# Kernel optimization log

Hardware: AMD Instinct MI355X
Metric: run time of the kernel (lower is better)

## Reference

```python
import jax, jax.numpy as jnp
import numpy as np

N_HEAD = 16
HEAD_DIM = 32          # n_embed // n_head // 2
LAMBDA_INIT = 0.2      # 0.8 - 0.6*exp(-0.3*(layer-1)) with layer=1
ROPE_BASE = 10000.0
EPS = 1e-5


def _rope(x):
    # torchtune RotaryPositionalEmbeddings: interleaved adjacent pairs
    B, T, H, D = x.shape
    half = D // 2
    theta = ROPE_BASE ** (-(jnp.arange(half, dtype=jnp.float32) * 2.0 / D))  # [half]
    ang = jnp.arange(T, dtype=jnp.float32)[:, None] * theta[None, :]         # [T, half]
    cos = jnp.cos(ang)[None, :, None, :]
    sin = jnp.sin(ang)[None, :, None, :]
    xr = x.reshape(B, T, H, half, 2)
    x1, x2 = xr[..., 0], xr[..., 1]
    out = jnp.stack([x1 * cos - x2 * sin, x1 * sin + x2 * cos], axis=-1)
    return out.reshape(B, T, H, D).astype(x.dtype)


def reference(x, W_attn, W_proj, lambda_q1, lambda_k1, lambda_q2, lambda_k2):
    B, T, C = x.shape
    H, D = N_HEAD, HEAD_DIM
    qkv = x @ W_attn                              # [B,T,3C]
    q, k, v = jnp.split(qkv, 3, axis=-1)
    q = _rope(q.reshape(B, T, 2 * H, D)).transpose(0, 2, 1, 3)   # [B,2H,T,D]
    k = _rope(k.reshape(B, T, 2 * H, D)).transpose(0, 2, 1, 3)   # [B,2H,T,D]
    v = v.reshape(B, T, H, 2 * D).transpose(0, 2, 1, 3)          # [B,H,T,2D]

    lam = (jnp.exp(jnp.dot(lambda_q1, lambda_k1))
           - jnp.exp(jnp.dot(lambda_q2, lambda_k2)) + LAMBDA_INIT)

    # causal SDPA over both score paths (2H heads) in one pass, shared V
    scale = 1.0 / jnp.sqrt(jnp.asarray(D, x.dtype))
    scores = jnp.einsum('bhqd,bhkd->bhqk', q, k) * scale         # [B,2H,T,T]
    causal = jnp.tril(jnp.ones((T, T), dtype=bool))
    scores = jnp.where(causal, scores, jnp.finfo(scores.dtype).min)
    probs = jax.nn.softmax(scores, axis=-1)
    vv = jnp.concatenate([v, v], axis=1)                         # [B,2H,T,2D]
    A = jnp.einsum('bhqk,bhkd->bhqd', probs, vv)                 # [B,2H,T,2D]
    A1, A2 = A[:, :H], A[:, H:]

    diff = A1 - lam * A2                                         # [B,H,T,2D]
    # RMSNorm over last dim (2*head_dim), no affine, eps=1e-5
    diff = diff * jax.lax.rsqrt(jnp.mean(diff * diff, axis=-1, keepdims=True) + EPS)
    diff = (1.0 - LAMBDA_INIT) * diff
    out = diff.transpose(0, 2, 1, 3).reshape(B, T, C)
    return out @ W_proj


def setup_inputs() -> dict:
    key = jax.random.key(0)
    ks = jax.random.split(key, 7)
    B, T, C, D = 2, 2048, 1024, HEAD_DIM
    return {
        'x': jax.random.normal(ks[0], (B, T, C), jnp.float32),
        'W_attn': jax.random.normal(ks[1], (C, 3 * C), jnp.float32) * 0.02,
        'W_proj': jax.random.normal(ks[2], (C, C), jnp.float32) * 0.02,
        'lambda_q1': jax.random.normal(ks[3], (D,), jnp.float32) * 0.1,
        'lambda_k1': jax.random.normal(ks[4], (D,), jnp.float32) * 0.1,
        'lambda_q2': jax.random.normal(ks[5], (D,), jnp.float32) * 0.1,
        'lambda_k2': jax.random.normal(ks[6], (D,), jnp.float32) * 0.1,
    }
```

## Files before the change

kernel.cpp:

```cpp
#include <hip/hip_runtime.h>


typedef unsigned short u16;
typedef __bf16 bf16x8 __attribute__((ext_vector_type(8)));
typedef float f32x4 __attribute__((ext_vector_type(4)));
typedef float f32x16 __attribute__((ext_vector_type(16)));
typedef unsigned u32x2 __attribute__((ext_vector_type(2)));

__device__ __forceinline__ u16 f2bf(float f) {
  return __builtin_bit_cast(u16, (__bf16)f);
}
__device__ __forceinline__ float bf2f(u16 u) {
  return (float)__builtin_bit_cast(__bf16, u);
}
__device__ __forceinline__ unsigned pk2(float a, float b) {
  return (unsigned)f2bf(a) | ((unsigned)f2bf(b) << 16);
}

__device__ __forceinline__ void gload16(const u16* g, u16* l) {
  __builtin_amdgcn_global_load_lds(
      (const __attribute__((address_space(1))) unsigned int*)g,
      (__attribute__((address_space(3))) unsigned int*)l, 16, 0, 0);
}

__device__ __forceinline__ void trans_body(const float* __restrict__ in,
                                           u16* __restrict__ out, int R, int Cn,
                                           int bx, int by, float (*tile)[33],
                                           int tx, int ty) {
  const int c0 = bx * 32, r0 = by * 32;
#pragma unroll
  for (int rr = 0; rr < 4; ++rr)
    tile[ty + rr * 8][tx] = in[(size_t)(r0 + ty + rr * 8) * Cn + c0 + tx];
  __syncthreads();
#pragma unroll
  for (int rr = 0; rr < 4; ++rr)
    out[(size_t)(c0 + ty + rr * 8) * R + r0 + tx] = f2bf(tile[tx][ty + rr * 8]);
}

__global__ __launch_bounds__(256) void prep_kernel(
    const float* __restrict__ x, const float* __restrict__ Wa,
    const float* __restrict__ Wp, const float* __restrict__ lq1,
    const float* __restrict__ lk1, const float* __restrict__ lq2,
    const float* __restrict__ lk2, u16* __restrict__ xb, u16* __restrict__ WaT,
    u16* __restrict__ WpT, float2* __restrict__ Tab, float* __restrict__ lamp) {
  __shared__ float tile[32][33];
  const int id = blockIdx.x;
  const int tx = threadIdx.x & 31, ty = threadIdx.x >> 5;
  if (id < 4096) {
    const int i = id * 256 + threadIdx.x;
    float4 v = ((const float4*)x)[i];
    ushort4 o;
    o.x = f2bf(v.x); o.y = f2bf(v.y); o.z = f2bf(v.z); o.w = f2bf(v.w);
    ((ushort4*)xb)[i] = o;
  } else if (id < 7168) {
    const int t = id - 4096;
    trans_body(Wa, WaT, 1024, 3072, t % 96, t / 96, tile, tx, ty);
  } else if (id < 8192) {
    const int t = id - 7168;
    trans_body(Wp, WpT, 1024, 1024, t & 31, t >> 5, tile, tx, ty);
  } else if (id < 8320) {
    const int idx = (id - 8192) * 256 + threadIdx.x;
    const int t = idx >> 4, i = idx & 15;
    const float theta = exp2f(-0.83048202372184059f * (float)i);
    float sn, cs;
    sincosf((float)t * theta, &sn, &cs);
    Tab[idx] = make_float2(cs, sn);
  } else if (threadIdx.x == 0) {
    float d1 = 0.f, d2 = 0.f;
#pragma unroll
    for (int i = 0; i < 32; ++i) {
      d1 += lq1[i] * lk1[i];
      d2 += lq2[i] * lk2[i];
    }
    *lamp = expf(d1) - expf(d2) + 0.2f;
  }
}

__global__ __launch_bounds__(256, 6) void gemm_qkv_kernel(
    const u16* __restrict__ A, const u16* __restrict__ BT,
    u16* __restrict__ Q, u16* __restrict__ K, u16* __restrict__ VT,
    const float2* __restrict__ Tab) {
  const int Kdim = 1024;
  __shared__ u16 As[64 * 32];
  __shared__ u16 Bs[128 * 32];
  const int tid = threadIdx.x;
  const int l = tid & 63;
  const int w = tid >> 6;
  const int nwgx = gridDim.x;
  const int lin = blockIdx.x + nwgx * blockIdx.y;
  const int cpx = (nwgx * gridDim.y) >> 3;
  const int swz = (lin & 7) * cpx + (lin >> 3);
  const int bm = swz / nwgx, bn = swz % nwgx;
  const int wm = w >> 1, wn = w & 1;
  const int rowA0 = bm * 64, rowB0 = bn * 128;
  const int r_ = tid >> 2;
  const int s_ = (tid & 3) * 8;
  const u16* Ag = &A[(size_t)(rowA0 + r_) * Kdim + s_];
  const u16* Bg = &BT[(size_t)(rowB0 + r_) * Kdim + s_];
  const size_t rstride = (size_t)64 * Kdim;
  f32x4 acc[2][4] = {};
  for (int k0 = 0; k0 < Kdim; k0 += 32) {
    gload16(Ag + k0, &As[r_ * 32 + s_]);
    gload16(Bg + k0, &Bs[r_ * 32 + s_]);
    gload16(Bg + rstride + k0, &Bs[2048 + r_ * 32 + s_]);
    __syncthreads();
    bf16x8 a[2], b[4];
#pragma unroll
    for (int i = 0; i < 2; ++i)
      a[i] = *(const bf16x8*)&As[(wm * 32 + i * 16 + (l & 15)) * 32 + (l >> 4) * 8];
#pragma unroll
    for (int j = 0; j < 4; ++j)
      b[j] = *(const bf16x8*)&Bs[(wn * 64 + j * 16 + (l & 15)) * 32 + (l >> 4) * 8];
#pragma unroll
    for (int i = 0; i < 2; ++i)
#pragma unroll
      for (int j = 0; j < 4; ++j)
        acc[i][j] = __builtin_amdgcn_mfma_f32_16x16x32_bf16(a[i], b[j], acc[i][j], 0, 0, 0);
    __syncthreads();
  }
  const int cr = (l >> 4) * 4;
  const int cc = l & 15;
  const int region = bn >> 3;
  const int b_ = rowA0 >> 11, tb = rowA0 & 2047;
  if (region < 2) {
    const float qsc_ = (region == 0) ? 0.25503486f : 1.0f;
    u16* dst = (region == 0) ? Q : K;
#pragma unroll
    for (int i = 0; i < 2; ++i) {
      const int trow0 = wm * 32 + i * 16 + cr;
#pragma unroll
      for (int j = 0; j < 4; ++j) {
        const int c = (bn & 7) * 128 + wn * 64 + j * 16 + cc;
        const int hh = c >> 5, d = c & 31;
        const int ii = d >> 1;
        const float sgn = (d & 1) ? 1.0f : -1.0f;
        const size_t base = (size_t)(b_ * 32 + hh) * 2048;
#pragma unroll
        for (int r = 0; r < 4; ++r) {
          const int t = tb + trow0 + r;
          const float2 cs = Tab[t * 16 + ii];
          const float xv = acc[i][j][r];
          const float px = __shfl_xor(xv, 1, 64);
          dst[(base + t) * 32 + d] = f2bf((xv * cs.x + sgn * px * cs.y) * qsc_);
        }
      }
    }
  } else {
#pragma unroll
    for (int i = 0; i < 2; ++i) {
      const int t0 = tb + wm * 32 + i * 16 + cr;
#pragma unroll
      for (int j = 0; j < 4; ++j) {
        const int c3 = (bn & 7) * 128 + wn * 64 + j * 16 + cc;
        const int hv = c3 >> 6, dv = c3 & 63;
        ushort4 ov;
        ov.x = f2bf(acc[i][j][0]);
        ov.y = f2bf(acc[i][j][1]);
        ov.z = f2bf(acc[i][j][2]);
        ov.w = f2bf(acc[i][j][3]);
        *(ushort4*)&VT[((size_t)(b_ * 16 + hv) * 64 + dv) * 2048 + t0] = ov;
      }
    }
  }
}

__global__ __launch_bounds__(256) void gemm_out_kernel(
    const u16* __restrict__ A, const u16* __restrict__ BT, float* __restrict__ Cout,
    int Mdim, int Ndim, int Kdim) {
  __shared__ u16 As[64 * 32];
  __shared__ u16 Bs[128 * 32];
  const int tid = threadIdx.x;
  const int l = tid & 63;
  const int w = tid >> 6;
  const int nwgx = gridDim.x;
  const int lin = blockIdx.x + nwgx * blockIdx.y;
  const int cpx = (nwgx * gridDim.y) >> 3;
  const int swz = (lin & 7) * cpx + (lin >> 3);
  const int bm = swz / nwgx, bn = swz % nwgx;
  const int wm = w >> 1, wn = w & 1;
  const int rowA0 = bm * 64, rowB0 = bn * 128;
  const int r_ = tid >> 2;
  const int s_ = (tid & 3) * 8;
  const u16* Ag = &A[(size_t)(rowA0 + r_) * Kdim + s_];
  const u16* Bg = &BT[(size_t)(rowB0 + r_) * Kdim + s_];
  const size_t rstride = (size_t)64 * Kdim;
  f32x4 acc[2][4] = {};
  for (int k0 = 0; k0 < Kdim; k0 += 32) {
    gload16(Ag + k0, &As[r_ * 32 + s_]);
    gload16(Bg + k0, &Bs[r_ * 32 + s_]);
    gload16(Bg + rstride + k0, &Bs[2048 + r_ * 32 + s_]);
    __syncthreads();
    bf16x8 a[2], b[4];
#pragma unroll
    for (int i = 0; i < 2; ++i)
      a[i] = *(const bf16x8*)&As[(wm * 32 + i * 16 + (l & 15)) * 32 + (l >> 4) * 8];
#pragma unroll
    for (int j = 0; j < 4; ++j)
      b[j] = *(const bf16x8*)&Bs[(wn * 64 + j * 16 + (l & 15)) * 32 + (l >> 4) * 8];
#pragma unroll
    for (int i = 0; i < 2; ++i)
#pragma unroll
      for (int j = 0; j < 4; ++j)
        acc[i][j] = __builtin_amdgcn_mfma_f32_16x16x32_bf16(a[i], b[j], acc[i][j], 0, 0, 0);
    __syncthreads();
  }
  const int cr = (l >> 4) * 4;
  const int cc = l & 15;
#pragma unroll
  for (int i = 0; i < 2; ++i)
#pragma unroll
    for (int j = 0; j < 4; ++j)
#pragma unroll
      for (int r = 0; r < 4; ++r) {
        const int row = rowA0 + wm * 32 + i * 16 + cr + r;
        const int col = rowB0 + wn * 64 + j * 16 + cc;
        Cout[(size_t)row * Ndim + col] = acc[i][j][r];
      }
}

__global__ __launch_bounds__(256, 4) void attn_kernel(const u16* __restrict__ Q,
                                                      const u16* __restrict__ K,
                                                      const u16* __restrict__ VT,
                                                      u16* __restrict__ PO0,
                                                      u16* __restrict__ PO1,
                                                      float* __restrict__ ML) {
  __shared__ u16 Ks[64 * 34];
  __shared__ u16 Vs[64 * 66];
  __shared__ u16 Os[4 * 32 * 66];
  const int tid = threadIdx.x, l = tid & 63, w = tid >> 6;
  const int pp = blockIdx.x & 7, hf = blockIdx.x >> 3;
  const int h = blockIdx.y, b = blockIdx.z;
  const size_t qkbase = (size_t)(b * 32 + h) * 2048;
  const size_t vtb = (size_t)(b * 16 + (h & 15)) * 64;
  const int lq = l & 31, hi = l >> 5;
  const f32x16 z16 = {};
  const int krow = tid >> 2, ksl = (tid & 3) * 8;
  const int dva = tid >> 3, vsl = (tid & 7) * 8;
  const int dvb = dva + 32;
  const __bf16 one1 = (__bf16)1.0f;
  const bf16x8 ones = {one1, one1, one1, one1, one1, one1, one1, one1};

  for (int halfidx = 0; halfidx < 2; ++halfidx) {
    const int qt = halfidx ? (15 - pp) : pp;
    const int slot = hf ^ halfidx;
    const int s_begin = slot ? (qt + 1) : 0;
    const int s_end = slot ? (2 * qt + 2) : (qt + 1);
    const int q0 = qt * 128;
    const int qw = q0 + w * 32;
    const int q = qw + lq;
    const bf16x8 qf0 = *(const bf16x8*)&Q[(qkbase + q) * 32 + hi * 8];
    const bf16x8 qf1 = *(const bf16x8*)&Q[(qkbase + q) * 32 + 16 + hi * 8];
    f32x16 olo = {}, ohi = {}, lacc = {};
    uint4 kreg = *(const uint4*)&K[(qkbase + s_begin * 64 + krow) * 32 + ksl];
    uint4 vreg0 = *(const uint4*)&VT[(vtb + dva) * 2048 + s_begin * 64 + vsl];
    uint4 vreg1 = *(const uint4*)&VT[(vtb + dvb) * 2048 + s_begin * 64 + vsl];
    for (int s = s_begin; s < s_end; ++s) {
      const int kb = s * 64;
      *(uint4*)&Ks[krow * 34 + ksl] = kreg;
      *(uint4*)&Vs[dva * 66 + vsl] = vreg0;
      *(uint4*)&Vs[dvb * 66 + vsl] = vreg1;
      const int sn = (s + 1 < s_end) ? (s + 1) : s;
      kreg = *(const uint4*)&K[(qkbase + sn * 64 + krow) * 32 + ksl];
      vreg0 = *(const uint4*)&VT[(vtb + dva) * 2048 + sn * 64 + vsl];
      vreg1 = *(const uint4*)&VT[(vtb + dvb) * 2048 + sn * 64 + vsl];
      __syncthreads();
      if (qw + 31 >= kb) {
        f32x16 s0_, s1_;
        {
          const bf16x8 ka0 = *(const bf16x8*)&Ks[lq * 34 + hi * 8];
          const bf16x8 ka1 = *(const bf16x8*)&Ks[lq * 34 + 16 + hi * 8];
          const bf16x8 kc0 = *(const bf16x8*)&Ks[(32 + lq) * 34 + hi * 8];
          const bf16x8 kc1 = *(const bf16x8*)&Ks[(32 + lq) * 34 + 16 + hi * 8];
          __builtin_amdgcn_s_setprio(1);
          s0_ = __builtin_amdgcn_mfma_f32_32x32x16_bf16(ka0, qf0, z16, 0, 0, 0);
          s0_ = __builtin_amdgcn_mfma_f32_32x32x16_bf16(ka1, qf1, s0_, 0, 0, 0);
          s1_ = __builtin_amdgcn_mfma_f32_32x32x16_bf16(kc0, qf0, z16, 0, 0, 0);
          s1_ = __builtin_amdgcn_mfma_f32_32x32x16_bf16(kc1, qf1, s1_, 0, 0, 0);
          __builtin_amdgcn_s_setprio(0);
        }
        const bool nm = (kb + 63 > qw);
        if (nm) {
#pragma unroll
          for (int r = 0; r < 16; ++r) {
            const int kr = (r & 3) + 8 * (r >> 2) + 4 * hi;
            if (kb + kr > q) s0_[r] = -1e30f;
            if (kb + 32 + kr > q) s1_[r] = -1e30f;
          }
        }
#pragma unroll
        for (int r = 0; r < 16; ++r) {
          s0_[r] = __builtin_amdgcn_exp2f(s0_[r]);
          s1_[r] = __builtin_amdgcn_exp2f(s1_[r]);
        }
        unsigned pw[16];
#pragma unroll
        for (int j = 0; j < 8; ++j) {
          pw[j] = pk2(s0_[2 * j], s0_[2 * j + 1]);
          pw[8 + j] = pk2(s1_[2 * j], s1_[2 * j + 1]);
        }
        bf16x8 pa[4];
#pragma unroll
        for (int fidx = 0; fidx < 4; ++fidx) {
          const unsigned* wt = &pw[fidx * 4];
          union { unsigned u[4]; bf16x8 v; } fr;
#if __has_builtin(__builtin_amdgcn_permlane32_swap)
          const u32x2 rA = __builtin_amdgcn_permlane32_swap(wt[0], wt[2], false, false);
          const u32x2 rB = __builtin_amdgcn_permlane32_swap(wt[1], wt[3], false, false);
          fr.u[0] = rA[0]; fr.u[1] = rB[0]; fr.u[2] = rA[1]; fr.u[3] = rB[1];
#else
          const unsigned ua = hi ? wt[0] : wt[2];
          const unsigned ub = hi ? wt[1] : wt[3];
          const unsigned sa = __shfl_xor(ua, 32, 64);
          const unsigned sb = __shfl_xor(ub, 32, 64);
          fr.u[0] = hi ? sa : wt[0];
          fr.u[1] = hi ? sb : wt[1];
          fr.u[2] = hi ? wt[2] : sa;
          fr.u[3] = hi ? wt[3] : sb;
#endif
          pa[fidx] = fr.v;
        }
        __builtin_amdgcn_s_setprio(1);
#pragma unroll
        for (int ks = 0; ks < 4; ++ks) {
          const bf16x8 va = *(const bf16x8*)&Vs[lq * 66 + ks * 16 + hi * 8];
          const bf16x8 vb = *(const bf16x8*)&Vs[(32 + lq) * 66 + ks * 16 + hi * 8];
          olo = __builtin_amdgcn_mfma_f32_32x32x16_bf16(va, pa[ks], olo, 0, 0, 0);
          ohi = __builtin_amdgcn_mfma_f32_32x32x16_bf16(vb, pa[ks], ohi, 0, 0, 0);
          lacc = __builtin_amdgcn_mfma_f32_32x32x16_bf16(ones, pa[ks], lacc, 0, 0, 0);
        }
        __builtin_amdgcn_s_setprio(0);
      }
      __syncthreads();
    }
    const float lsum = lacc[0];
    const float inv = (lsum > 0.f) ? (1.0f / lsum) : 0.f;
    if (hi == 0)
      ML[(size_t)slot * 131072 + qkbase + q] = lsum;
    u16* Ow = &Os[(w * 32 + lq) * 66];
#pragma unroll
    for (int g = 0; g < 4; ++g) {
      const int d0 = 8 * g + 4 * hi;
      *(unsigned*)&Ow[d0] = pk2(olo[4 * g] * inv, olo[4 * g + 1] * inv);
      *(unsigned*)&Ow[d0 + 2] = pk2(olo[4 * g + 2] * inv, olo[4 * g + 3] * inv);
      *(unsigned*)&Ow[32 + d0] = pk2(ohi[4 * g] * inv, ohi[4 * g + 1] * inv);
      *(unsigned*)&Ow[32 + d0 + 2] = pk2(ohi[4 * g + 2] * inv, ohi[4 * g + 3] * inv);
    }
    __syncthreads();
    u16* PO = slot ? PO1 : PO0;
    for (int s2 = tid; s2 < 1024; s2 += 256) {
      const int wv = s2 >> 8, qq = (s2 >> 3) & 31, sl = (s2 & 7) * 8;
      *(uint4*)&PO[(qkbase + q0 + wv * 32 + qq) * 64 + sl] =
          *(const uint4*)&Os[(wv * 32 + qq) * 66 + sl];
    }
    __syncthreads();
  }
}

__global__ __launch_bounds__(256) void diff_rms_kernel(
    const u16* __restrict__ PO0, const u16* __restrict__ PO1,
    const float* __restrict__ ML, const float* __restrict__ lamp,
    u16* __restrict__ Mb) {
  const int g = threadIdx.x >> 5;
  const int dl = (threadIdx.x & 31) * 2;
  const int ridx = blockIdx.x * 8 + g;
  const int b = ridx >> 15, rem = ridx & 32767, h = rem >> 11, t = rem & 2047;
  const float lam = *lamp;
  const size_t row1 = (size_t)(b * 32 + h) * 2048 + t;
  const size_t row2 = (size_t)(b * 32 + 16 + h) * 2048 + t;
  const float lA1 = ML[row1], lB1 = ML[131072 + row1];
  const float lA2 = ML[row2], lB2 = ML[131072 + row2];
  const float i1 = 1.0f / (lA1 + lB1);
  const float wa1 = lA1 * i1, wb1 = lB1 * i1;
  const float i2 = 1.0f / (lA2 + lB2);
  const float wa2 = lA2 * i2, wb2 = lB2 * i2;
  const ushort2 p01 = *(const ushort2*)&PO0[row1 * 64 + dl];
  const ushort2 p11 = *(const ushort2*)&PO1[row1 * 64 + dl];
  const ushort2 p02 = *(const ushort2*)&PO0[row2 * 64 + dl];
  const ushort2 p12 = *(const ushort2*)&PO1[row2 * 64 + dl];
  const float a1x = wa1 * bf2f(p01.x) + wb1 * bf2f(p11.x);
  const float a1y = wa1 * bf2f(p01.y) + wb1 * bf2f(p11.y);
  const float a2x = wa2 * bf2f(p02.x) + wb2 * bf2f(p12.x);
  const float a2y = wa2 * bf2f(p02.y) + wb2 * bf2f(p12.y);
  const float df0 = a1x - lam * a2x;
  const float df1 = a1y - lam * a2y;
  float ss = df0 * df0 + df1 * df1;
  ss += __shfl_xor(ss, 1, 64);
  ss += __shfl_xor(ss, 2, 64);
  ss += __shfl_xor(ss, 4, 64);
  ss += __shfl_xor(ss, 8, 64);
  ss += __shfl_xor(ss, 16, 64);
  const float rms = rsqrtf(ss * (1.0f / 64.0f) + 1e-5f);
  ushort2 o;
  o.x = f2bf(0.8f * df0 * rms);
  o.y = f2bf(0.8f * df1 * rms);
  *(ushort2*)&Mb[((size_t)(b * 2048 + t)) * 1024 + h * 64 + dl] = o;
}

extern "C" void kernel_launch(void* const* d_in, const int* in_sizes, int n_in,
                              void* d_out, int out_size, void* d_ws, size_t ws_size,
                              hipStream_t stream) {
  const float* x = (const float*)d_in[0];
  const float* Wa = (const float*)d_in[1];
  const float* Wp = (const float*)d_in[2];
  const float* lq1 = (const float*)d_in[3];
  const float* lk1 = (const float*)d_in[4];
  const float* lq2 = (const float*)d_in[5];
  const float* lk2 = (const float*)d_in[6];
  if (ws_size < (size_t)(64u << 20)) return;

  char* ws = (char*)d_ws;
  u16* Qarr = (u16*)(ws);
  u16* Karr = (u16*)(ws + (8u << 20));
  u16* VTarr = (u16*)(ws + (16u << 20));
  u16* WpT = (u16*)(ws + (24u << 20));
  char* arena = ws + (26u << 20);
  u16* xb = (u16*)(arena);
  u16* WaT = (u16*)(arena + (8u << 20));
  float2* Tab = (float2*)(arena + (14u << 20));
  u16* PO0 = (u16*)(arena);
  u16* PO1 = (u16*)(arena + (16u << 20));
  float* ML = (float*)(arena + (32u << 20));
  float* lamp = (float*)(arena + (33u << 20));
  u16* Mbuf = Qarr;

  prep_kernel<<<8321, 256, 0, stream>>>(x, Wa, Wp, lq1, lk1, lq2, lk2,
                                        xb, WaT, WpT, Tab, lamp);
  gemm_qkv_kernel<<<dim3(24, 64), 256, 0, stream>>>(xb, WaT, Qarr, Karr, VTarr, Tab);
  attn_kernel<<<dim3(16, 32, 2), 256, 0, stream>>>(Qarr, Karr, VTarr, PO0, PO1, ML);
  diff_rms_kernel<<<8192, 256, 0, stream>>>(PO0, PO1, ML, lamp, Mbuf);
  gemm_out_kernel<<<dim3(8, 64), 256, 0, stream>>>(Mbuf, WpT, (float*)d_out, 4096, 1024, 1024);
}
```

Baseline: 142.5 us.

## Double-buffer LDS tiles in QKV and output GEMMs to overlap loads

Both GEMM kernels now keep two LDS stages and prefetch the next K-slice with global_load_lds while computing MFMAs on the current one. This removes one of the two barriers per iteration and is meant to hide global load latency behind compute. MFMA sections are also raised in wave priority with s_setprio. LDS use doubles to 24 KB per block, which may reduce occupancy. The global_load_lds writes may not be waited on correctly before the barrier, so the prefetch depends on the compiler inserting the right vmcnt waits.

Result: faster. 138.6 us (-2.8%).

```diff
diff --git a/kernel.cpp b/kernel.cpp
--- a/kernel.cpp
+++ b/kernel.cpp
@@ -81,8 +81,7 @@
     u16* __restrict__ Q, u16* __restrict__ K, u16* __restrict__ VT,
     const float2* __restrict__ Tab) {
   const int Kdim = 1024;
-  __shared__ u16 As[64 * 32];
-  __shared__ u16 Bs[128 * 32];
+  __shared__ u16 SH[12288];
   const int tid = threadIdx.x;
   const int l = tid & 63;
   const int w = tid >> 6;
@@ -99,24 +98,37 @@
   const u16* Bg = &BT[(size_t)(rowB0 + r_) * Kdim + s_];
   const size_t rstride = (size_t)64 * Kdim;
   f32x4 acc[2][4] = {};
-  for (int k0 = 0; k0 < Kdim; k0 += 32) {
-    gload16(Ag + k0, &As[r_ * 32 + s_]);
-    gload16(Bg + k0, &Bs[r_ * 32 + s_]);
-    gload16(Bg + rstride + k0, &Bs[2048 + r_ * 32 + s_]);
-    __syncthreads();
+  gload16(Ag, &SH[tid * 8]);
+  gload16(Bg, &SH[2048 + tid * 8]);
+  gload16(Bg + rstride, &SH[4096 + tid * 8]);
+  __syncthreads();
+  int cur = 0;
+  for (int t = 0; t < 32; ++t) {
+    const u16* Asc = SH + cur * 6144;
+    const u16* Bsc = Asc + 2048;
+    if (t + 1 < 32) {
+      u16* Asn = SH + (cur ^ 1) * 6144;
+      const int k1 = (t + 1) * 32;
+      gload16(Ag + k1, &Asn[tid * 8]);
+      gload16(Bg + k1, &Asn[2048 + tid * 8]);
+      gload16(Bg + rstride + k1, &Asn[4096 + tid * 8]);
+    }
     bf16x8 a[2], b[4];
 #pragma unroll
     for (int i = 0; i < 2; ++i)
-      a[i] = *(const bf16x8*)&As[(wm * 32 + i * 16 + (l & 15)) * 32 + (l >> 4) * 8];
+      a[i] = *(const bf16x8*)&Asc[(wm * 32 + i * 16 + (l & 15)) * 32 + (l >> 4) * 8];
 #pragma unroll
     for (int j = 0; j < 4; ++j)
-      b[j] = *(const bf16x8*)&Bs[(wn * 64 + j * 16 + (l & 15)) * 32 + (l >> 4) * 8];
+      b[j] = *(const bf16x8*)&Bsc[(wn * 64 + j * 16 + (l & 15)) * 32 + (l >> 4) * 8];
+    __builtin_amdgcn_s_setprio(1);
 #pragma unroll
     for (int i = 0; i < 2; ++i)
 #pragma unroll
       for (int j = 0; j < 4; ++j)
         acc[i][j] = __builtin_amdgcn_mfma_f32_16x16x32_bf16(a[i], b[j], acc[i][j], 0, 0, 0);
+    __builtin_amdgcn_s_setprio(0);
     __syncthreads();
+    cur ^= 1;
   }
   const int cr = (l >> 4) * 4;
   const int cc = l & 15;
@@ -167,8 +179,7 @@
 __global__ __launch_bounds__(256) void gemm_out_kernel(
     const u16* __restrict__ A, const u16* __restrict__ BT, float* __restrict__ Cout,
     int Mdim, int Ndim, int Kdim) {
-  __shared__ u16 As[64 * 32];
-  __shared__ u16 Bs[128 * 32];
+  __shared__ u16 SH[12288];
   const int tid = threadIdx.x;
   const int l = tid & 63;
   const int w = tid >> 6;
@@ -185,24 +196,38 @@
   const u16* Bg = &BT[(size_t)(rowB0 + r_) * Kdim + s_];
   const size_t rstride = (size_t)64 * Kdim;
   f32x4 acc[2][4] = {};
-  for (int k0 = 0; k0 < Kdim; k0 += 32) {
-    gload16(Ag + k0, &As[r_ * 32 + s_]);
-    gload16(Bg + k0, &Bs[r_ * 32 + s_]);
-    gload16(Bg + rstride + k0, &Bs[2048 + r_ * 32 + s_]);
-    __syncthreads();
+  gload16(Ag, &SH[tid * 8]);
+  gload16(Bg, &SH[2048 + tid * 8]);
+  gload16(Bg + rstride, &SH[4096 + tid * 8]);
+  __syncthreads();
+  int cur = 0;
+  const int nt = Kdim >> 5;
+  for (int t = 0; t < nt; ++t) {
+    const u16* Asc = SH + cur * 6144;
+    const u16* Bsc = Asc + 2048;
+    if (t + 1 < nt) {
+      u16* Asn = SH + (cur ^ 1) * 6144;
+      const int k1 = (t + 1) * 32;
+      gload16(Ag + k1, &Asn[tid * 8]);
+      gload16(Bg + k1, &Asn[2048 + tid * 8]);
+      gload16(Bg + rstride + k1, &Asn[4096 + tid * 8]);
+    }
     bf16x8 a[2], b[4];
 #pragma unroll
     for (int i = 0; i < 2; ++i)
-      a[i] = *(const bf16x8*)&As[(wm * 32 + i * 16 + (l & 15)) * 32 + (l >> 4) * 8];
+      a[i] = *(const bf16x8*)&Asc[(wm * 32 + i * 16 + (l & 15)) * 32 + (l >> 4) * 8];
 #pragma unroll
     for (int j = 0; j < 4; ++j)
-      b[j] = *(const bf16x8*)&Bs[(wn * 64 + j * 16 + (l & 15)) * 32 + (l >> 4) * 8];
+      b[j] = *(const bf16x8*)&Bsc[(wn * 64 + j * 16 + (l & 15)) * 32 + (l >> 4) * 8];
+    __builtin_amdgcn_s_setprio(1);
 #pragma unroll
     for (int i = 0; i < 2; ++i)
 #pragma unroll
       for (int j = 0; j < 4; ++j)
         acc[i][j] = __builtin_amdgcn_mfma_f32_16x16x32_bf16(a[i], b[j], acc[i][j], 0, 0, 0);
+    __builtin_amdgcn_s_setprio(0);
     __syncthreads();
+    cur ^= 1;
   }
   const int cr = (l >> 4) * 4;
   const int cc = l & 15;
```
